# Kernel tuning notes

Hardware: AMD Instinct MI355X
Metric: run time of the kernel (lower is better)

The kernel has to match this reference:

```python
import math
import jax, jax.numpy as jnp
import numpy as np

TAU = 2.0
ALPHA = math.exp(-1.0 / TAU)
SCALE = 1.0

T, B, H, N, D = 16, 16, 8, 256, 64


def setup_inputs() -> dict:
    key = jax.random.key(0)
    x = jax.random.normal(key, (T, B, H, N, D), dtype=jnp.float32)
    return {"x": x}


def reference(x):
    # state_t = alpha * state_{t-1} + x_t  (state_0-init = 0)
    # out_t   = x_t * sigmoid(scale * state_t)
    def step(state, xt):
        state = ALPHA * state + xt
        return state, xt * jax.nn.sigmoid(SCALE * state)

    init = jnp.zeros_like(x[0])  # [B, H, N, D]
    _, out = jax.lax.scan(step, init, x)  # out: [T, B, H, N, D]
    return out
```

## Files before the change

### kernel.cpp

```cpp
#include <hip/hip_runtime.h>


#define T_STEPS 16
#define SPATIAL (16LL * 8LL * 256LL * 64LL)
#define VEC4    (SPATIAL / 4)
#define ALPHA_F 0.60653065971263342f

typedef float f32x4 __attribute__((ext_vector_type(4)));

__global__ __launch_bounds__(256) void
TemporalPSPGate_35613868819159_kernel(const f32x4* __restrict__ x,
                                      f32x4* __restrict__ out) {
    const long long i = (long long)blockIdx.x * 256 + threadIdx.x;

    f32x4 xv[T_STEPS];
    #pragma unroll
    for (int t = 0; t < T_STEPS; ++t) {
        xv[t] = __builtin_nontemporal_load(x + (long long)t * VEC4 + i);
    }

    f32x4 st = {0.f, 0.f, 0.f, 0.f};
    #pragma unroll
    for (int t = 0; t < T_STEPS; ++t) {
        st = ALPHA_F * st + xv[t];

        f32x4 o;
        #pragma unroll
        for (int c = 0; c < 4; ++c) {
            const float e = __expf(-st[c]);
            o[c] = xv[t][c] * __builtin_amdgcn_rcpf(1.0f + e);
        }
        __builtin_nontemporal_store(o, out + (long long)t * VEC4 + i);
    }
}

extern "C" void kernel_launch(void* const* d_in, const int* in_sizes, int n_in,
                              void* d_out, int out_size, void* d_ws, size_t ws_size,
                              hipStream_t stream) {
    const f32x4* x = (const f32x4*)d_in[0];
    f32x4* out = (f32x4*)d_out;

    const int block = 256;
    const int grid = (int)(VEC4 / block);

    TemporalPSPGate_35613868819159_kernel<<<grid, block, 0, stream>>>(x, out);
}
```

Baseline: 227.9 us.

## Process four columns per thread with two-step prefetch ring and regular stores

Each thread now handles four vec4 columns strided by 64 within its wave, and the grid shrinks by the same factor. Instead of loading all 16 timesteps up front, the kernel keeps a two-timestep register ring and issues loads for step t+2 while computing step t. Output stores switch from nontemporal to regular stores. This is meant to overlap loads with compute and stores while keeping register use bounded, at the cost of fewer loads in flight per thread at kernel start and fewer blocks overall.

Result: faster. 217.6 us (-4.5%).

```diff
diff --git a/kernel.cpp b/kernel.cpp
--- a/kernel.cpp
+++ b/kernel.cpp
@@ -5,32 +5,57 @@
 #define SPATIAL (16LL * 8LL * 256LL * 64LL)
 #define VEC4    (SPATIAL / 4)
 #define ALPHA_F 0.60653065971263342f
+#define SUB     4
 
 typedef float f32x4 __attribute__((ext_vector_type(4)));
 
 __global__ __launch_bounds__(256) void
 TemporalPSPGate_35613868819159_kernel(const f32x4* __restrict__ x,
                                       f32x4* __restrict__ out) {
-    const long long i = (long long)blockIdx.x * 256 + threadIdx.x;
+    const int tid  = threadIdx.x;
+    const int wave = tid >> 6;
+    const int lane = tid & 63;
+    const long long wb = ((long long)blockIdx.x * 4 + wave) * 256;
+    const long long j  = wb + lane;
 
-    f32x4 xv[T_STEPS];
+    f32x4 xv[2][SUB];
+    #pragma unroll
+    for (int tt = 0; tt < 2; ++tt)
+        #pragma unroll
+        for (int s = 0; s < SUB; ++s)
+            xv[tt][s] = __builtin_nontemporal_load(
+                x + (long long)tt * VEC4 + j + 64 * s);
+
+    f32x4 st[SUB];
+    #pragma unroll
+    for (int s = 0; s < SUB; ++s) st[s] = (f32x4){0.f, 0.f, 0.f, 0.f};
+
     #pragma unroll
     for (int t = 0; t < T_STEPS; ++t) {
-        xv[t] = __builtin_nontemporal_load(x + (long long)t * VEC4 + i);
-    }
+        const int cur = t & 1;
 
-    f32x4 st = {0.f, 0.f, 0.f, 0.f};
-    #pragma unroll
-    for (int t = 0; t < T_STEPS; ++t) {
-        st = ALPHA_F * st + xv[t];
+        f32x4 xt[SUB];
+        #pragma unroll
+        for (int s = 0; s < SUB; ++s) xt[s] = xv[cur][s];
 
-        f32x4 o;
+        if (t + 2 < T_STEPS) {
+            #pragma unroll
+            for (int s = 0; s < SUB; ++s)
+                xv[cur][s] = __builtin_nontemporal_load(
+                    x + (long long)(t + 2) * VEC4 + j + 64 * s);
+        }
+
         #pragma unroll
-        for (int c = 0; c < 4; ++c) {
-            const float e = __expf(-st[c]);
-            o[c] = xv[t][c] * __builtin_amdgcn_rcpf(1.0f + e);
+        for (int s = 0; s < SUB; ++s) {
+            st[s] = ALPHA_F * st[s] + xt[s];
+            f32x4 o;
+            #pragma unroll
+            for (int c = 0; c < 4; ++c) {
+                const float e = __expf(-st[s][c]);
+                o[c] = xt[s][c] * __builtin_amdgcn_rcpf(1.0f + e);
+            }
+            out[(long long)t * VEC4 + j + 64 * s] = o;
         }
-        __builtin_nontemporal_store(o, out + (long long)t * VEC4 + i);
     }
 }
 
@@ -41,7 +66,7 @@
     f32x4* out = (f32x4*)d_out;
 
     const int block = 256;
-    const int grid = (int)(VEC4 / block);
+    const int grid = (int)(VEC4 / (block * SUB));
 
     TemporalPSPGate_35613868819159_kernel<<<grid, block, 0, stream>>>(x, out);
 }
```

## Process eight vectors per thread with double-buffered timestep prefetch

Applied to the files above, without the earlier changes.

Each thread now handles eight float4 columns, spaced 64 apart within its wave, instead of one, and the grid shrinks by a factor of eight. Timestep loads are double-buffered two steps ahead rather than loading all sixteen steps up front, so memory loads overlap with the sigmoid math. Stores also switch from nontemporal to regular stores. The per-thread register footprint grows (four arrays of eight float4), which may lower occupancy, and far fewer waves are launched to hide memory latency.

Measured after the change: 231.4 us. Within noise of the previous version (+1.6%).

```diff
diff --git a/kernel.cpp b/kernel.cpp
--- a/kernel.cpp
+++ b/kernel.cpp
@@ -5,33 +5,59 @@
 #define SPATIAL (16LL * 8LL * 256LL * 64LL)
 #define VEC4    (SPATIAL / 4)
 #define ALPHA_F 0.60653065971263342f
+#define SUB     8
 
 typedef float f32x4 __attribute__((ext_vector_type(4)));
 
 __global__ __launch_bounds__(256) void
 TemporalPSPGate_35613868819159_kernel(const f32x4* __restrict__ x,
                                       f32x4* __restrict__ out) {
-    const long long i = (long long)blockIdx.x * 256 + threadIdx.x;
+    const int tid  = threadIdx.x;
+    const int wave = tid >> 6;
+    const int lane = tid & 63;
+    const long long wb = ((long long)blockIdx.x * 4 + wave) * (64 * SUB);
+    const long long j  = wb + lane;
 
-    f32x4 xv[T_STEPS];
+    f32x4 bufA[SUB], bufB[SUB], xt[SUB], st[SUB];
+
     #pragma unroll
-    for (int t = 0; t < T_STEPS; ++t) {
-        xv[t] = __builtin_nontemporal_load(x + (long long)t * VEC4 + i);
+    for (int s = 0; s < SUB; ++s)
+        bufA[s] = __builtin_nontemporal_load(x + j + 64 * s);
+    #pragma unroll
+    for (int s = 0; s < SUB; ++s)
+        bufB[s] = __builtin_nontemporal_load(x + VEC4 + j + 64 * s);
+    #pragma unroll
+    for (int s = 0; s < SUB; ++s) st[s] = (f32x4){0.f, 0.f, 0.f, 0.f};
+
+    #define STEP(T, CURBUF)                                                   \
+    {                                                                         \
+        _Pragma("unroll")                                                     \
+        for (int s = 0; s < SUB; ++s) xt[s] = CURBUF[s];                      \
+        if ((T) + 2 < T_STEPS) {                                              \
+            _Pragma("unroll")                                                 \
+            for (int s = 0; s < SUB; ++s)                                     \
+                CURBUF[s] = __builtin_nontemporal_load(                       \
+                    x + (long long)((T) + 2) * VEC4 + j + 64 * s);            \
+        }                                                                     \
+        _Pragma("unroll")                                                     \
+        for (int s = 0; s < SUB; ++s) {                                       \
+            st[s] = ALPHA_F * st[s] + xt[s];                                  \
+            f32x4 o;                                                          \
+            _Pragma("unroll")                                                 \
+            for (int c = 0; c < 4; ++c) {                                     \
+                const float e = __expf(-st[s][c]);                            \
+                o[c] = xt[s][c] * __builtin_amdgcn_rcpf(1.0f + e);            \
+            }                                                                 \
+            out[(long long)(T) * VEC4 + j + 64 * s] = o;                      \
+        }                                                                     \
     }
 
-    f32x4 st = {0.f, 0.f, 0.f, 0.f};
     #pragma unroll
-    for (int t = 0; t < T_STEPS; ++t) {
-        st = ALPHA_F * st + xv[t];
-
-        f32x4 o;
-        #pragma unroll
-        for (int c = 0; c < 4; ++c) {
-            const float e = __expf(-st[c]);
-            o[c] = xv[t][c] * __builtin_amdgcn_rcpf(1.0f + e);
-        }
-        __builtin_nontemporal_store(o, out + (long long)t * VEC4 + i);
+    for (int tt = 0; tt < T_STEPS; tt += 2) {
+        STEP(tt,     bufA);
+        STEP(tt + 1, bufB);
     }
+    #undef STEP
 }
 
 extern "C" void kernel_launch(void* const* d_in, const int* in_sizes, int n_in,
@@ -41,7 +67,7 @@
     f32x4* out = (f32x4*)d_out;
 
     const int block = 256;
-    const int grid = (int)(VEC4 / block);
+    const int grid = (int)(VEC4 / (block * SUB));
 
     TemporalPSPGate_35613868819159_kernel<<<grid, block, 0, stream>>>(x, out);
 }
```
